# Kernel tuning notes

Measured on AMD Instinct MI355X. Metric: run time of the kernel, lower is better.

Reference implementation:

```python
import jax, jax.numpy as jnp
import numpy as np

B, T, DM, H, R = 2, 2048, 1024, 16, 8
HD = DM // H
LORA_SCALE = 16.0 / R  # alpha / r


def setup_inputs() -> dict:
    key = jax.random.key(0)
    ks = jax.random.split(key, 8)
    return {
        "hidden_states": jax.random.normal(ks[0], (B, T, DM), jnp.float32),
        "attention_mask": jnp.zeros((B, 1, 1, T), jnp.float32),
        "Wq": jax.random.normal(ks[1], (DM, DM), jnp.float32) * 0.02,
        "bq": jnp.zeros((DM,), jnp.float32),
        "Aq": jax.random.normal(ks[2], (R, DM), jnp.float32) * 0.02,
        "Bq": jax.random.normal(ks[3], (DM, R), jnp.float32) * 0.02,
        "Wk": jax.random.normal(ks[4], (DM, DM), jnp.float32) * 0.02,
        "bk": jnp.zeros((DM,), jnp.float32),
        "Wv": jax.random.normal(ks[5], (DM, DM), jnp.float32) * 0.02,
        "bv": jnp.zeros((DM,), jnp.float32),
        "Av": jax.random.normal(ks[6], (R, DM), jnp.float32) * 0.02,
        "Bv": jax.random.normal(ks[7], (DM, R), jnp.float32) * 0.02,
    }


def _lora_linear(x, W, b, A, Bmat):
    # y = x W^T + b + scale * (x A^T) B^T   (lora_dropout = 0 in eval)
    return x @ W.T + b + LORA_SCALE * ((x @ A.T) @ Bmat.T)


def _heads(x):
    # [b, t, (h d)] -> [b, h, t, d]
    b, t, _ = x.shape
    return x.reshape(b, t, H, HD).transpose(0, 2, 1, 3)


def reference(hidden_states, attention_mask, Wq, bq, Aq, Bq, Wk, bk, Wv, bv, Av, Bv):
    q = _heads(_lora_linear(hidden_states, Wq, bq, Aq, Bq))
    k = _heads(hidden_states @ Wk.T + bk)
    v = _heads(_lora_linear(hidden_states, Wv, bv, Av, Bv))

    scores = jnp.einsum("bhtd,bhsd->bhts", q, k) * (HD ** -0.5)
    causal = jnp.triu(jnp.ones((T, T), dtype=bool), k=1)[None, None]
    scores = jnp.where(causal, jnp.float32(-jnp.inf), scores)
    scores = scores + attention_mask
    probs = jax.nn.softmax(scores, axis=-1)  # dropout p=0 (eval)
    attn = jnp.einsum("bhts,bhsd->bhtd", probs, v)
    # [b, h, t, d] -> [b, t, h*d]
    return attn.transpose(0, 2, 1, 3).reshape(B, T, DM)
```

## Files before the change

kernel.cpp:

```cpp
#include <hip/hip_runtime.h>
#include <hip/hip_bf16.h>

#define BB 2
#define TT 2048
#define DMM 1024
#define HH 16
#define HDD 64

typedef __attribute__((ext_vector_type(8))) short bf16x8;
typedef __attribute__((ext_vector_type(4))) short short4v;
typedef __attribute__((ext_vector_type(4))) float f32x4;

static __device__ __forceinline__ short f2bf(float f) {
    __hip_bfloat16 h = __float2bfloat16(f);
    return *reinterpret_cast<short*>(&h);
}

static __device__ __forceinline__ float ex2(float x) {
    return __builtin_amdgcn_exp2f(x);
}

static __device__ __forceinline__ void gl_lds16(const void* g, void* l) {
    __builtin_amdgcn_global_load_lds(
        (const __attribute__((address_space(1))) void*)g,
        (__attribute__((address_space(3))) void*)l, 16, 0, 0);
}

__global__ void cvt_hidden(const float* __restrict__ x, short* __restrict__ y) {
    int i = blockIdx.x * 256 + threadIdx.x;
    float4 v = reinterpret_cast<const float4*>(x)[i];
    short4v o;
    o[0] = f2bf(v.x); o[1] = f2bf(v.y); o[2] = f2bf(v.z); o[3] = f2bf(v.w);
    reinterpret_cast<short4v*>(y)[i] = o;
}

__global__ void prep_w(const float* __restrict__ Wq, const float* __restrict__ Aq, const float* __restrict__ Bq,
                       const float* __restrict__ Wk,
                       const float* __restrict__ Wv, const float* __restrict__ Av, const float* __restrict__ Bv,
                       short* __restrict__ Wqe, short* __restrict__ Wke, short* __restrict__ Wve) {
    const int mode = blockIdx.y;
    const float* W = (mode == 0) ? Wq : (mode == 1) ? Wk : Wv;
    const float* A = (mode == 0) ? Aq : Av;
    const float* Bm = (mode == 0) ? Bq : Bv;
    short* outp = (mode == 0) ? Wqe : (mode == 1) ? Wke : Wve;
    int idx = blockIdx.x * 256 + threadIdx.x;
    int n = idx >> 10, k = idx & 1023;
    float v = W[idx];
    if (mode != 1) {
        float s = 0.f;
#pragma unroll
        for (int r = 0; r < 8; ++r) s += Bm[n * 8 + r] * A[r * 1024 + k];
        v += 2.0f * s;
    }
    outp[idx] = f2bf(v);
}

__global__ __launch_bounds__(256, 5) void proj_gemm(
        const short* __restrict__ Xbf,
        const short* __restrict__ Wq, const short* __restrict__ Wk, const short* __restrict__ Wv,
        const float* __restrict__ bq, const float* __restrict__ bk, const float* __restrict__ bv,
        short* __restrict__ Qb, short* __restrict__ Kb, short* __restrict__ Vtb) {
    __shared__ __align__(16) char As[64 * 128];
    __shared__ __align__(16) char Bs[128 * 128];

    const int mode = blockIdx.z;
    const short* Wbf = (mode == 0) ? Wq : (mode == 1) ? Wk : Wv;
    const float* bias = (mode == 0) ? bq : (mode == 1) ? bk : bv;
    short* outp = (mode == 0) ? Qb : (mode == 1) ? Kb : Vtb;
    const float scale = (mode == 0) ? 0.18033688f : 1.0f;

    const int tid = threadIdx.x;
    const int wave = tid >> 6, lane = tid & 63;
    const int l15 = lane & 15, l4 = lane >> 4;
    const int bx = blockIdx.x, by = blockIdx.y;
    const int wx = 2 * (bx & 3) + (by & 1);
    const int wy = (bx >> 2) * 32 + (by >> 1);
    const int m0 = wy * 64, n0 = wx * 128;
    const int wm = (wave >> 1) * 32, wn = (wave & 1) * 64;

    const int lrow8 = lane >> 3;
    const int lchunk = lane & 7;
    const int srcoff = (lchunk ^ lrow8) * 8;
    char* ldsA = As + wave * 2048;
    char* ldsB = Bs + wave * 4096;

#define PROJ_STAGE(K0) do {                                                          \
    _Pragma("unroll")                                                                \
    for (int i = 0; i < 2; ++i)                                                      \
        gl_lds16(Xbf + (m0 + wave * 16 + i * 8 + lrow8) * 1024 + (K0) + srcoff,      \
                 ldsA + i * 1024);                                                   \
    _Pragma("unroll")                                                                \
    for (int i = 0; i < 4; ++i)                                                      \
        gl_lds16(Wbf + (n0 + wave * 32 + i * 8 + lrow8) * 1024 + (K0) + srcoff,      \
                 ldsB + i * 1024);                                                   \
} while (0)

#define PROJ_FRAGS(KK)                                                               \
    const int colb = (KK) * 64 + l4 * 16;                                            \
    bf16x8 wf[4], xf[2];                                                             \
    _Pragma("unroll")                                                                \
    for (int w = 0; w < 4; ++w) {                                                    \
        int r = wn + w * 16 + l15;                                                   \
        wf[w] = *reinterpret_cast<const bf16x8*>(Bs + ((r * 128 + colb) ^ ((r & 7) << 4))); \
    }                                                                                \
    _Pragma("unroll")                                                                \
    for (int x = 0; x < 2; ++x) {                                                    \
        int r = wm + x * 16 + l15;                                                   \
        xf[x] = *reinterpret_cast<const bf16x8*>(As + ((r * 128 + colb) ^ ((r & 7) << 4))); \
    }

    if (mode != 2) {
        f32x4 acc[4][2] = {};
        for (int k0 = 0; k0 < 1024; k0 += 64) {
            __syncthreads();
            PROJ_STAGE(k0);
            __syncthreads();
#pragma unroll
            for (int kk = 0; kk < 2; ++kk) {
                PROJ_FRAGS(kk);
#pragma unroll
                for (int w = 0; w < 4; ++w)
#pragma unroll
                    for (int x = 0; x < 2; ++x)
                        acc[w][x] = __builtin_amdgcn_mfma_f32_16x16x32_bf16(wf[w], xf[x], acc[w][x], 0, 0, 0);
            }
        }
#pragma unroll
        for (int w = 0; w < 4; ++w) {
            int gnb = n0 + wn + w * 16 + l4 * 4;
            int hh = gnb >> 6, d = gnb & 63;
            float4 bv4 = *reinterpret_cast<const float4*>(bias + gnb);
#pragma unroll
            for (int x = 0; x < 2; ++x) {
                int gm = m0 + wm + x * 16 + l15;
                int bb = gm >> 11, t = gm & 2047;
                short4v o;
                o[0] = f2bf((acc[w][x][0] + bv4.x) * scale);
                o[1] = f2bf((acc[w][x][1] + bv4.y) * scale);
                o[2] = f2bf((acc[w][x][2] + bv4.z) * scale);
                o[3] = f2bf((acc[w][x][3] + bv4.w) * scale);
                *reinterpret_cast<short4v*>(outp + ((bb * 16 + hh) * 2048 + t) * 64 + d) = o;
            }
        }
    } else {
        f32x4 acc[2][4] = {};
        for (int k0 = 0; k0 < 1024; k0 += 64) {
            __syncthreads();
            PROJ_STAGE(k0);
            __syncthreads();
#pragma unroll
            for (int kk = 0; kk < 2; ++kk) {
                PROJ_FRAGS(kk);
#pragma unroll
                for (int x = 0; x < 2; ++x)
#pragma unroll
                    for (int w = 0; w < 4; ++w)
                        acc[x][w] = __builtin_amdgcn_mfma_f32_16x16x32_bf16(xf[x], wf[w], acc[x][w], 0, 0, 0);
            }
        }
#pragma unroll
        for (int x = 0; x < 2; ++x) {
            int gmb = m0 + wm + x * 16 + l4 * 4;
            int bb = gmb >> 11, t = gmb & 2047;
#pragma unroll
            for (int w = 0; w < 4; ++w) {
                int gn = n0 + wn + w * 16 + l15;
                int hh = gn >> 6, d = gn & 63;
                int tx = ((gn >> 3) & 1) << 2;
                float bvs = bias[gn];
                short4v o;
                o[0] = f2bf(acc[x][w][0] + bvs);
                o[1] = f2bf(acc[x][w][1] + bvs);
                o[2] = f2bf(acc[x][w][2] + bvs);
                o[3] = f2bf(acc[x][w][3] + bvs);
                *reinterpret_cast<short4v*>(outp + ((bb * 16 + hh) * 64 + d) * 2048 + (t ^ tx)) = o;
            }
        }
    }
}


#define STAGE(BUF, T) do {                                                           \
    const int _kv = (T) << 5;                                                        \
    gl_lds16(Kp + (_kv + krow) * 64 + kswz, MEM + (BUF) * 4096 + wv * 1024);         \
    gl_lds16(Vp + lane * 2048 + _kv + wv * 8, MEM + 16384 + (BUF) * 4096 + wv * 1024);\
} while (0)

#define SLICEJOB(QF0, QF1, OO, M, L, QBASE) do {                                     \
    f32x4 ss = {};                                                                   \
    ss = __builtin_amdgcn_mfma_f32_16x16x32_bf16(kf0, QF0, ss, 0, 0, 0);             \
    ss = __builtin_amdgcn_mfma_f32_16x16x32_bf16(kf1, QF1, ss, 0, 0, 0);             \
    float pr[4];                                                                     \
    if (kvs + 15 > (QBASE)) {                                                        \
        _Pragma("unroll")                                                            \
        for (int r = 0; r < 4; ++r) {                                                \
            float v = ss[r] + mv[r];                                                 \
            if (kvs + l4*4 + r > (QBASE) + l15) v = -1e30f;                          \
            pr[r] = v;                                                               \
        }                                                                            \
    } else {                                                                         \
        _Pragma("unroll")                                                            \
        for (int r = 0; r < 4; ++r) pr[r] = ss[r] + mv[r];                           \
    }                                                                                \
    float tl = fmaxf(fmaxf(pr[0], pr[1]), fmaxf(pr[2], pr[3]));                      \
    if (!__all(tl - (M) <= 11.5415603f)) {                                           \
        float tm = tl;                                                               \
        tm = fmaxf(tm, __shfl_xor(tm, 16));                                          \
        tm = fmaxf(tm, __shfl_xor(tm, 32));                                          \
        float mn = fmaxf((M), tm);                                                   \
        float al = ex2((M) - mn);                                                    \
        M = mn; L *= al;                                                             \
        _Pragma("unroll")                                                            \
        for (int dt = 0; dt < 4; ++dt)                                               \
            _Pragma("unroll")                                                        \
            for (int r = 0; r < 4; ++r) OO[dt][r] *= al;                             \
    }                                                                                \
    _Pragma("unroll")                                                                \
    for (int r = 0; r < 4; ++r) pr[r] = ex2(pr[r] - (M));                            \
    L += (pr[0] + pr[1]) + (pr[2] + pr[3]);                                          \
    short4v pa;                                                                      \
    _Pragma("unroll")                                                                \
    for (int r = 0; r < 4; ++r) pa[r] = f2bf(pr[r]);                                 \
    _Pragma("unroll")                                                                \
    for (int dt = 0; dt < 4; ++dt)                                                   \
        OO[dt] = __builtin_amdgcn_mfma_f32_16x16x16bf16_1k(vf[dt], pa, OO[dt], 0, 0, 0); \
} while (0)

__global__ __launch_bounds__(256, 4) void attn(
        const short* __restrict__ Qb, const short* __restrict__ Kb,
        const short* __restrict__ Vt, const float* __restrict__ amask,
        float* __restrict__ outp) {
    __shared__ __align__(16) char MEM[40960];

    const int tid = threadIdx.x, wv = tid >> 6, lane = tid & 63;
    const int l15 = lane & 15, l4 = lane >> 4;
    const int xcd = blockIdx.x & 7;
    const int k   = blockIdx.x >> 3;
    const int j   = ((k >> 5) << 3) | ((k & 3) << 1) | ((k >> 4) & 1);
    const int bh  = xcd * 4 + ((k >> 2) & 3);
    const int p  = wv & 1;
    const int s  = wv >> 1;
    const int i  = 2 * j + p;
    const int b = bh >> 4, h = bh & 15;

    const short* Qp = Qb + bh * TT * HDD;
    const short* Kp = Kb + bh * TT * HDD;
    const short* Vp = Vt + bh * HDD * TT;
    const float* mp = amask + b * TT;
    float* mlds = (float*)(MEM + 32768);

    const int qbaseA = (127 - i) << 4;
    const int qbaseB = i << 4;
    const int nkA = ((qbaseA + 15 - 16 * s) >> 5) + 1;
    const int nkB = ((qbaseB + 15 - 16 * s) >> 5) + 1;
    const int NT = ((127 - 2 * j) * 16 + 47) >> 5;

    const int krow = wv * 8 + (lane >> 3);
    const int kswz = ((lane & 7) ^ (lane >> 3)) * 8;

    const int kb0 = (16 * s + l15) * 128 + ((l4 ^ (l15 & 7)) << 4);
    const int vb0 = (2 * s + (l4 >> 1)) * 1024 + l15 * 16 + (((l4 & 1) ^ (l15 >> 3)) << 3);

    {
        int mi8 = tid * 8;
        float4 a = *reinterpret_cast<const float4*>(mp + mi8);
        float4 c = *reinterpret_cast<const float4*>(mp + mi8 + 4);
        a.x *= 1.44269504f; a.y *= 1.44269504f; a.z *= 1.44269504f; a.w *= 1.44269504f;
        c.x *= 1.44269504f; c.y *= 1.44269504f; c.z *= 1.44269504f; c.w *= 1.44269504f;
        *reinterpret_cast<float4*>(mlds + mi8) = a;
        *reinterpret_cast<float4*>(mlds + mi8 + 4) = c;
    }

    bf16x8 qfA0 = *reinterpret_cast<const bf16x8*>(Qp + (qbaseA + l15) * 64 + l4 * 8);
    bf16x8 qfA1 = *reinterpret_cast<const bf16x8*>(Qp + (qbaseA + l15) * 64 + 32 + l4 * 8);
    bf16x8 qfB0 = *reinterpret_cast<const bf16x8*>(Qp + (qbaseB + l15) * 64 + l4 * 8);
    bf16x8 qfB1 = *reinterpret_cast<const bf16x8*>(Qp + (qbaseB + l15) * 64 + 32 + l4 * 8);

    f32x4 OA[4] = {}, OB[4] = {};
    float MA = -1e30f, LA = 0.f, MB = -1e30f, LB = 0.f;

    STAGE(0, 0);
    STAGE(1, 1);
    asm volatile("s_waitcnt lgkmcnt(0)" ::: "memory");

    int cur = 0;
    for (int t = 0; t < NT; ++t) {
        if (t + 2 < NT) {
            int nb = cur + 2; if (nb >= 4) nb -= 4;
            STAGE(nb, t + 2);
            asm volatile("s_waitcnt vmcnt(4)" ::: "memory");
        } else if (t + 1 < NT) {
            asm volatile("s_waitcnt vmcnt(2)" ::: "memory");
        } else {
            asm volatile("s_waitcnt vmcnt(0)" ::: "memory");
        }
        asm volatile("s_barrier" ::: "memory");
        if (t < nkA) {
            const char* Kcur = MEM + cur * 4096;
            const char* Vcur = MEM + 16384 + cur * 4096;
            bf16x8 kf0 = *reinterpret_cast<const bf16x8*>(Kcur + kb0);
            bf16x8 kf1 = *reinterpret_cast<const bf16x8*>(Kcur + (kb0 ^ 64));
            short4v vf[4];
#pragma unroll
            for (int dt = 0; dt < 4; ++dt)
                vf[dt] = *reinterpret_cast<const short4v*>(Vcur + vb0 + dt * 256);
            const int kvs = (t << 5) + 16 * s;
            float4 mv = *reinterpret_cast<const float4*>(mlds + kvs + l4 * 4);
            SLICEJOB(qfA0, qfA1, OA, MA, LA, qbaseA);
            if (t < nkB) SLICEJOB(qfB0, qfB1, OB, MB, LB, qbaseB);
        }
        ++cur; if (cur == 4) cur = 0;
    }
    asm volatile("s_barrier" ::: "memory");

    LA += __shfl_xor(LA, 16); LA += __shfl_xor(LA, 32);
    LB += __shfl_xor(LB, 16); LB += __shfl_xor(LB, 32);

    float* mg = (float*)MEM + p * 2560 + lane * 40;
    if (s) {
#pragma unroll
        for (int dt = 0; dt < 4; ++dt) *reinterpret_cast<f32x4*>(mg + dt * 4) = OA[dt];
        mg[16] = MA; mg[17] = LA;
#pragma unroll
        for (int dt = 0; dt < 4; ++dt) *reinterpret_cast<f32x4*>(mg + 20 + dt * 4) = OB[dt];
        mg[36] = MB; mg[37] = LB;
    }
    __syncthreads();
    if (!s) {
        {
            float m1 = mg[16], l1 = mg[17];
            float ms = fmaxf(MA, m1);
            float e0 = ex2(MA - ms), e1 = ex2(m1 - ms);
            float inv = 1.0f / (LA * e0 + l1 * e1);
            int tA = qbaseA + l15;
#pragma unroll
            for (int dt = 0; dt < 4; ++dt) {
                f32x4 o1 = *reinterpret_cast<const f32x4*>(mg + dt * 4);
                float4 o;
                o.x = (OA[dt][0] * e0 + o1[0] * e1) * inv;
                o.y = (OA[dt][1] * e0 + o1[1] * e1) * inv;
                o.z = (OA[dt][2] * e0 + o1[2] * e1) * inv;
                o.w = (OA[dt][3] * e0 + o1[3] * e1) * inv;
                *reinterpret_cast<float4*>(outp + (b * 2048 + tA) * 1024 + h * 64 + dt * 16 + l4 * 4) = o;
            }
        }
        {
            float m1 = mg[36], l1 = mg[37];
            float ms = fmaxf(MB, m1);
            float e0 = ex2(MB - ms), e1 = ex2(m1 - ms);
            float inv = 1.0f / (LB * e0 + l1 * e1);
            int tB = qbaseB + l15;
#pragma unroll
            for (int dt = 0; dt < 4; ++dt) {
                f32x4 o1 = *reinterpret_cast<const f32x4*>(mg + 20 + dt * 4);
                float4 o;
                o.x = (OB[dt][0] * e0 + o1[0] * e1) * inv;
                o.y = (OB[dt][1] * e0 + o1[1] * e1) * inv;
                o.z = (OB[dt][2] * e0 + o1[2] * e1) * inv;
                o.w = (OB[dt][3] * e0 + o1[3] * e1) * inv;
                *reinterpret_cast<float4*>(outp + (b * 2048 + tB) * 1024 + h * 64 + dt * 16 + l4 * 4) = o;
            }
        }
    }
}

extern "C" void kernel_launch(void* const* d_in, const int* in_sizes, int n_in,
                              void* d_out, int out_size, void* d_ws, size_t ws_size,
                              hipStream_t stream) {
    const float* hidden = (const float*)d_in[0];
    const float* amask  = (const float*)d_in[1];
    const float* Wq = (const float*)d_in[2];
    const float* bq = (const float*)d_in[3];
    const float* Aq = (const float*)d_in[4];
    const float* Bq = (const float*)d_in[5];
    const float* Wk = (const float*)d_in[6];
    const float* bk = (const float*)d_in[7];
    const float* Wv = (const float*)d_in[8];
    const float* bv = (const float*)d_in[9];
    const float* Av = (const float*)d_in[10];
    const float* Bv = (const float*)d_in[11];
    float* outp = (float*)d_out;

    char* ws = (char*)d_ws;
    short* Xbf = (short*)(ws);
    short* Wqe = (short*)(ws + (8 << 20));
    short* Wke = (short*)(ws + (10 << 20));
    short* Wve = (short*)(ws + (12 << 20));
    short* Qb  = (short*)(ws + (14 << 20));
    short* Kb  = (short*)(ws + (22 << 20));
    short* Vtb = (short*)(ws + (30 << 20));

    cvt_hidden<<<4096, 256, 0, stream>>>(hidden, Xbf);
    prep_w<<<dim3(4096, 3), 256, 0, stream>>>(Wq, Aq, Bq, Wk, Wv, Av, Bv, Wqe, Wke, Wve);
    proj_gemm<<<dim3(8, 64, 3), 256, 0, stream>>>(Xbf, Wqe, Wke, Wve, bq, bk, bv, Qb, Kb, Vtb);
    attn<<<1024, 256, 0, stream>>>(Qb, Kb, Vtb, amask, outp);
}
```

Measured before the change: 104.4 us.

## Double-buffer projection GEMM LDS tiles and unroll attention ring-buffer loop

The projection GEMM now uses two LDS buffers, so the global-to-LDS load for the next K tile is issued before the MFMAs on the current tile, with one barrier per step instead of two. The launch-bounds occupancy hint drops from 5 to 3 blocks because LDS use doubles to 48KB per block. The attention main loop is unrolled by four so the ring-buffer slot index becomes a compile-time constant, removing the runtime buffer-index arithmetic. The main risks are lower occupancy and larger code in the proj kernel.

```diff
diff --git a/kernel.cpp b/kernel.cpp
--- a/kernel.cpp
+++ b/kernel.cpp
@@ -55,13 +55,13 @@
     outp[idx] = f2bf(v);
 }
 
-__global__ __launch_bounds__(256, 5) void proj_gemm(
+__global__ __launch_bounds__(256, 3) void proj_gemm(
         const short* __restrict__ Xbf,
         const short* __restrict__ Wq, const short* __restrict__ Wk, const short* __restrict__ Wv,
         const float* __restrict__ bq, const float* __restrict__ bk, const float* __restrict__ bv,
         short* __restrict__ Qb, short* __restrict__ Kb, short* __restrict__ Vtb) {
-    __shared__ __align__(16) char As[64 * 128];
-    __shared__ __align__(16) char Bs[128 * 128];
+    __shared__ __align__(16) char As[2][64 * 128];
+    __shared__ __align__(16) char Bs[2][128 * 128];
 
     const int mode = blockIdx.z;
     const short* Wbf = (mode == 0) ? Wq : (mode == 1) ? Wk : Wv;
@@ -81,49 +81,67 @@
     const int lrow8 = lane >> 3;
     const int lchunk = lane & 7;
     const int srcoff = (lchunk ^ lrow8) * 8;
-    char* ldsA = As + wave * 2048;
-    char* ldsB = Bs + wave * 4096;
-
-#define PROJ_STAGE(K0) do {                                                          \
+
+#define PROJ_STAGE(BUF, K0) do {                                                     \
     _Pragma("unroll")                                                                \
     for (int i = 0; i < 2; ++i)                                                      \
         gl_lds16(Xbf + (m0 + wave * 16 + i * 8 + lrow8) * 1024 + (K0) + srcoff,      \
-                 ldsA + i * 1024);                                                   \
+                 As[BUF] + wave * 2048 + i * 1024);                                  \
     _Pragma("unroll")                                                                \
     for (int i = 0; i < 4; ++i)                                                      \
         gl_lds16(Wbf + (n0 + wave * 32 + i * 8 + lrow8) * 1024 + (K0) + srcoff,      \
-                 ldsB + i * 1024);                                                   \
-} while (0)
-
-#define PROJ_FRAGS(KK)                                                               \
+                 Bs[BUF] + wave * 4096 + i * 1024);                                  \
+} while (0)
+
+#define PROJ_FRAGS(BUF, KK)                                                          \
     const int colb = (KK) * 64 + l4 * 16;                                            \
     bf16x8 wf[4], xf[2];                                                             \
     _Pragma("unroll")                                                                \
     for (int w = 0; w < 4; ++w) {                                                    \
         int r = wn + w * 16 + l15;                                                   \
-        wf[w] = *reinterpret_cast<const bf16x8*>(Bs + ((r * 128 + colb) ^ ((r & 7) << 4))); \
+        wf[w] = *reinterpret_cast<const bf16x8*>(Bs[BUF] + ((r * 128 + colb) ^ ((r & 7) << 4))); \
     }                                                                                \
     _Pragma("unroll")                                                                \
     for (int x = 0; x < 2; ++x) {                                                    \
         int r = wm + x * 16 + l15;                                                   \
-        xf[x] = *reinterpret_cast<const bf16x8*>(As + ((r * 128 + colb) ^ ((r & 7) << 4))); \
-    }
+        xf[x] = *reinterpret_cast<const bf16x8*>(As[BUF] + ((r * 128 + colb) ^ ((r & 7) << 4))); \
+    }
+
+#define PROJ_MFMA_T(BUF) do {                                                        \
+    _Pragma("unroll")                                                                \
+    for (int kk = 0; kk < 2; ++kk) {                                                 \
+        PROJ_FRAGS(BUF, kk);                                                         \
+        _Pragma("unroll")                                                            \
+        for (int w = 0; w < 4; ++w)                                                  \
+            _Pragma("unroll")                                                        \
+            for (int x = 0; x < 2; ++x)                                              \
+                acc[w][x] = __builtin_amdgcn_mfma_f32_16x16x32_bf16(wf[w], xf[x], acc[w][x], 0, 0, 0); \
+    }                                                                                \
+} while (0)
+
+#define PROJ_MFMA_N(BUF) do {                                                        \
+    _Pragma("unroll")                                                                \
+    for (int kk = 0; kk < 2; ++kk) {                                                 \
+        PROJ_FRAGS(BUF, kk);                                                         \
+        _Pragma("unroll")                                                            \
+        for (int x = 0; x < 2; ++x)                                                  \
+            _Pragma("unroll")                                                        \
+            for (int w = 0; w < 4; ++w)                                              \
+                acc[x][w] = __builtin_amdgcn_mfma_f32_16x16x32_bf16(xf[x], wf[w], acc[x][w], 0, 0, 0); \
+    }                                                                                \
+} while (0)
 
     if (mode != 2) {
         f32x4 acc[4][2] = {};
-        for (int k0 = 0; k0 < 1024; k0 += 64) {
+        PROJ_STAGE(0, 0);
+        __syncthreads();
+        for (int t = 0; t < 16; t += 2) {
+            PROJ_STAGE(1, (t + 1) * 64);
+            PROJ_MFMA_T(0);
             __syncthreads();
-            PROJ_STAGE(k0);
+            if (t + 2 < 16) PROJ_STAGE(0, (t + 2) * 64);
+            PROJ_MFMA_T(1);
             __syncthreads();
-#pragma unroll
-            for (int kk = 0; kk < 2; ++kk) {
-                PROJ_FRAGS(kk);
-#pragma unroll
-                for (int w = 0; w < 4; ++w)
-#pragma unroll
-                    for (int x = 0; x < 2; ++x)
-                        acc[w][x] = __builtin_amdgcn_mfma_f32_16x16x32_bf16(wf[w], xf[x], acc[w][x], 0, 0, 0);
-            }
         }
 #pragma unroll
         for (int w = 0; w < 4; ++w) {
@@ -144,19 +162,15 @@
         }
     } else {
         f32x4 acc[2][4] = {};
-        for (int k0 = 0; k0 < 1024; k0 += 64) {
+        PROJ_STAGE(0, 0);
+        __syncthreads();
+        for (int t = 0; t < 16; t += 2) {
+            PROJ_STAGE(1, (t + 1) * 64);
+            PROJ_MFMA_N(0);
             __syncthreads();
-            PROJ_STAGE(k0);
+            if (t + 2 < 16) PROJ_STAGE(0, (t + 2) * 64);
+            PROJ_MFMA_N(1);
             __syncthreads();
-#pragma unroll
-            for (int kk = 0; kk < 2; ++kk) {
-                PROJ_FRAGS(kk);
-#pragma unroll
-                for (int x = 0; x < 2; ++x)
-#pragma unroll
-                    for (int w = 0; w < 4; ++w)
-                        acc[x][w] = __builtin_amdgcn_mfma_f32_16x16x32_bf16(xf[x], wf[w], acc[x][w], 0, 0, 0);
-            }
         }
 #pragma unroll
         for (int x = 0; x < 2; ++x) {
@@ -226,6 +240,32 @@
         OO[dt] = __builtin_amdgcn_mfma_f32_16x16x16bf16_1k(vf[dt], pa, OO[dt], 0, 0, 0); \
 } while (0)
 
+#define AITER(BUF, T) do {                                                           \
+    if ((T) + 2 < NT) {                                                              \
+        STAGE((((BUF) + 2) & 3), (T) + 2);                                           \
+        asm volatile("s_waitcnt vmcnt(4)" ::: "memory");                             \
+    } else if ((T) + 1 < NT) {                                                       \
+        asm volatile("s_waitcnt vmcnt(2)" ::: "memory");                             \
+    } else {                                                                         \
+        asm volatile("s_waitcnt vmcnt(0)" ::: "memory");                             \
+    }                                                                                \
+    asm volatile("s_barrier" ::: "memory");                                          \
+    if ((T) < nkA) {                                                                 \
+        const char* Kcur = MEM + (BUF) * 4096;                                       \
+        const char* Vcur = MEM + 16384 + (BUF) * 4096;                               \
+        bf16x8 kf0 = *reinterpret_cast<const bf16x8*>(Kcur + kb0);                   \
+        bf16x8 kf1 = *reinterpret_cast<const bf16x8*>(Kcur + (kb0 ^ 64));            \
+        short4v vf[4];                                                               \
+        _Pragma("unroll")                                                            \
+        for (int dt = 0; dt < 4; ++dt)                                               \
+            vf[dt] = *reinterpret_cast<const short4v*>(Vcur + vb0 + dt * 256);       \
+        const int kvs = ((T) << 5) + 16 * s;                                         \
+        float4 mv = *reinterpret_cast<const float4*>(mlds + kvs + l4 * 4);           \
+        SLICEJOB(qfA0, qfA1, OA, MA, LA, qbaseA);                                    \
+        if ((T) < nkB) SLICEJOB(qfB0, qfB1, OB, MB, LB, qbaseB);                     \
+    }                                                                                \
+} while (0)
+
 __global__ __launch_bounds__(256, 4) void attn(
         const short* __restrict__ Qb, const short* __restrict__ Kb,
         const short* __restrict__ Vt, const float* __restrict__ amask,
@@ -283,34 +323,15 @@
     STAGE(1, 1);
     asm volatile("s_waitcnt lgkmcnt(0)" ::: "memory");
 
-    int cur = 0;
-    for (int t = 0; t < NT; ++t) {
-        if (t + 2 < NT) {
-            int nb = cur + 2; if (nb >= 4) nb -= 4;
-            STAGE(nb, t + 2);
-            asm volatile("s_waitcnt vmcnt(4)" ::: "memory");
-        } else if (t + 1 < NT) {
-            asm volatile("s_waitcnt vmcnt(2)" ::: "memory");
-        } else {
-            asm volatile("s_waitcnt vmcnt(0)" ::: "memory");
-        }
-        asm volatile("s_barrier" ::: "memory");
-        if (t < nkA) {
-            const char* Kcur = MEM + cur * 4096;
-            const char* Vcur = MEM + 16384 + cur * 4096;
-            bf16x8 kf0 = *reinterpret_cast<const bf16x8*>(Kcur + kb0);
-            bf16x8 kf1 = *reinterpret_cast<const bf16x8*>(Kcur + (kb0 ^ 64));
-            short4v vf[4];
-#pragma unroll
-            for (int dt = 0; dt < 4; ++dt)
-                vf[dt] = *reinterpret_cast<const short4v*>(Vcur + vb0 + dt * 256);
-            const int kvs = (t << 5) + 16 * s;
-            float4 mv = *reinterpret_cast<const float4*>(mlds + kvs + l4 * 4);
-            SLICEJOB(qfA0, qfA1, OA, MA, LA, qbaseA);
-            if (t < nkB) SLICEJOB(qfB0, qfB1, OB, MB, LB, qbaseB);
-        }
-        ++cur; if (cur == 4) cur = 0;
-    }
+    int t = 0;
+    for (; t + 4 <= NT; t += 4) {
+        AITER(0, t);
+        AITER(1, t + 1);
+        AITER(2, t + 2);
+        AITER(3, t + 3);
+    }
+    for (; t < NT; ++t) AITER((t & 3), t);
+
     asm volatile("s_barrier" ::: "memory");
 
     LA += __shfl_xor(LA, 16); LA += __shfl_xor(LA, 32);
```

Measured after the change: 104.2 us. No clear change (-0.1%).
